# Kernel tuning notes

Measured on AMD Instinct MI355X. Metric: run time of the kernel, lower is better.

The kernel has to match this reference:

```python
import jax, jax.numpy as jnp
import numpy as np

N, E, P = 50000, 1600000, 500000
IN_DIM, HID, OUT = 512, 128, 64
EPS = 1e-5


def setup_inputs() -> dict:
    key = jax.random.key(0)
    ks = jax.random.split(key, 16)
    d = {}
    d['x'] = jax.random.normal(ks[0], (N, IN_DIM), dtype=jnp.float32)
    d['ei'] = jax.random.randint(ks[1], (2, E), 0, N, dtype=jnp.int32)
    d['src'] = jax.random.randint(ks[2], (P,), 0, N, dtype=jnp.int32)
    d['dst'] = jax.random.randint(ks[3], (P,), 0, N, dtype=jnp.int32)
    # GCNConv layer 1 params
    d['W1'] = jax.random.normal(ks[4], (IN_DIM, HID), dtype=jnp.float32) / np.sqrt(IN_DIM)
    d['b1'] = jnp.zeros((HID,), jnp.float32)
    d['bn1_gamma'] = jnp.ones((HID,), jnp.float32)
    d['bn1_beta'] = jnp.zeros((HID,), jnp.float32)
    d['bn1_mean'] = jnp.zeros((HID,), jnp.float32)
    d['bn1_var'] = jnp.ones((HID,), jnp.float32)
    # GCNConv layer 2 params
    d['W2'] = jax.random.normal(ks[5], (HID, OUT), dtype=jnp.float32) / np.sqrt(HID)
    d['b2'] = jnp.zeros((OUT,), jnp.float32)
    d['bn2_gamma'] = jnp.ones((OUT,), jnp.float32)
    d['bn2_beta'] = jnp.zeros((OUT,), jnp.float32)
    d['bn2_mean'] = jnp.zeros((OUT,), jnp.float32)
    d['bn2_var'] = jnp.ones((OUT,), jnp.float32)
    # edge head MLP
    d['hW1'] = jax.random.normal(ks[6], (2 * OUT, OUT), dtype=jnp.float32) / np.sqrt(2 * OUT)
    d['hb1'] = jnp.zeros((OUT,), jnp.float32)
    d['hW2'] = jax.random.normal(ks[7], (OUT, 1), dtype=jnp.float32) / np.sqrt(OUT)
    d['hb2'] = jnp.zeros((1,), jnp.float32)
    return d


def gcn_conv(x, ei, W, b):
    """PyG-style GCNConv: add self-loops, symmetric deg^-1/2 normalization."""
    xw = x @ W  # [N, F]
    row, col = ei[0], ei[1]
    ones = jnp.ones((ei.shape[1],), x.dtype)
    deg = jax.ops.segment_sum(ones, col, num_segments=N) + 1.0  # +1 for self-loop
    dinv = jax.lax.rsqrt(deg)
    norm = dinv[row] * dinv[col]  # [E]
    agg = jax.ops.segment_sum(norm[:, None] * xw[row], col, num_segments=N)
    # self-loop contribution: dinv[i]^2 * xw[i]
    return agg + (dinv * dinv)[:, None] * xw + b


def bn_eval(x, gamma, beta, mean, var):
    return (x - mean) * jax.lax.rsqrt(var + EPS) * gamma + beta


def reference(x, ei, src, dst, W1, b1, bn1_gamma, bn1_beta, bn1_mean, bn1_var,
              W2, b2, bn2_gamma, bn2_beta, bn2_mean, bn2_var, hW1, hb1, hW2, hb2):
    h = jax.nn.relu(bn_eval(gcn_conv(x, ei, W1, b1), bn1_gamma, bn1_beta, bn1_mean, bn1_var))
    # dropout is identity in eval mode
    z = jax.nn.relu(bn_eval(gcn_conv(h, ei, W2, b2), bn2_gamma, bn2_beta, bn2_mean, bn2_var))
    pair = jnp.concatenate([z[src], z[dst]], axis=1)  # [P, 2*OUT]
    hmid = jax.nn.relu(pair @ hW1 + hb1)
    logits = hmid @ hW2 + hb2  # [P, 1]
    return jax.nn.sigmoid(logits).squeeze(-1)
```

## Files before the change

### kernel.cpp

```cpp
#include <hip/hip_runtime.h>
#include <math.h>


typedef __attribute__((ext_vector_type(8))) short short8x;
typedef __attribute__((ext_vector_type(4))) float f32x4;

__device__ __forceinline__ unsigned short f2bf(float f) {
  unsigned int u = __float_as_uint(f);
  unsigned int r = u + 0x7FFFu + ((u >> 16) & 1u);
  return (unsigned short)(r >> 16);
}
__device__ __forceinline__ float bf2f(unsigned short u) {
  return __uint_as_float(((unsigned int)u) << 16);
}


__global__ void zero_int_kernel(int* __restrict__ p, int n) {
  int i = blockIdx.x * blockDim.x + threadIdx.x;
  if (i < n) p[i] = 0;
}

__global__ void degree_hist_kernel(const int* __restrict__ col, int* __restrict__ deg, int E) {
  int i = blockIdx.x * blockDim.x + threadIdx.x;
  if (i < E) atomicAdd(&deg[col[i]], 1);
}

__global__ __launch_bounds__(256) void scan_blocksum_kernel(const int* __restrict__ deg,
                                                            int* __restrict__ bsum, int n) {
  __shared__ int ws[4];
  int base = blockIdx.x * 1024;
  int tid = threadIdx.x;
  int s = 0;
#pragma unroll
  for (int j = 0; j < 4; ++j) {
    int i = base + tid + j * 256;
    if (i < n) s += deg[i];
  }
#pragma unroll
  for (int d = 1; d < 64; d <<= 1) s += __shfl_xor(s, d, 64);
  if ((tid & 63) == 0) ws[tid >> 6] = s;
  __syncthreads();
  if (tid == 0) bsum[blockIdx.x] = ws[0] + ws[1] + ws[2] + ws[3];
}

__global__ __launch_bounds__(64) void scan_bsum_kernel(int* __restrict__ bsum, int nb,
                                                       int* __restrict__ total) {
  int lane = threadIdx.x;
  int v = (lane < nb) ? bsum[lane] : 0;
  int incl = v;
#pragma unroll
  for (int d = 1; d < 64; d <<= 1) {
    int t = __shfl_up(incl, d, 64);
    if (lane >= d) incl += t;
  }
  if (lane < nb) bsum[lane] = incl - v;
  if (lane == 63) *total = incl;
}

__global__ __launch_bounds__(256) void scan_final_kernel(const int* __restrict__ deg,
                                                         const int* __restrict__ bsum,
                                                         int* __restrict__ offs,
                                                         float* __restrict__ dinv, int n) {
  __shared__ int wsum[4];
  int tid = threadIdx.x;
  int lane = tid & 63;
  int wid = tid >> 6;
  int idx0 = blockIdx.x * 1024 + tid * 4;
  int v[4];
#pragma unroll
  for (int j = 0; j < 4; ++j) {
    int i = idx0 + j;
    v[j] = (i < n) ? deg[i] : 0;
  }
  int tsum = v[0] + v[1] + v[2] + v[3];
  int incl = tsum;
#pragma unroll
  for (int d = 1; d < 64; d <<= 1) {
    int t = __shfl_up(incl, d, 64);
    if (lane >= d) incl += t;
  }
  if (lane == 63) wsum[wid] = incl;
  __syncthreads();
  int woff = 0;
#pragma unroll
  for (int w = 0; w < 4; ++w)
    if (w < wid) woff += wsum[w];
  int run = woff + incl - tsum + bsum[blockIdx.x];
#pragma unroll
  for (int j = 0; j < 4; ++j) {
    int i = idx0 + j;
    if (i < n) {
      offs[i] = run;
      dinv[i] = rsqrtf((float)v[j] + 1.0f);
      run += v[j];
    }
  }
}

__global__ void bucket_init_kernel(const int* __restrict__ offs, const int* __restrict__ total,
                                   int* __restrict__ bcur, int* __restrict__ offs_n, int NBK) {
  int b = blockIdx.x * blockDim.x + threadIdx.x;
  if (b < NBK) bcur[b] = offs[b * 256];
  if (b == 0) *offs_n = *total;
}

__global__ __launch_bounds__(256) void binA_kernel(const int* __restrict__ row,
                                                   const int* __restrict__ col,
                                                   int* __restrict__ bcur,
                                                   unsigned int* __restrict__ staging, int E,
                                                   int NBK) {
  __shared__ int hist[256];
  const int tid = threadIdx.x;
  hist[tid] = 0;
  __syncthreads();
  const int base = blockIdx.x * 4096;
  unsigned int payload[16];
  int bk[16];
#pragma unroll
  for (int j = 0; j < 16; ++j) {
    int i = base + j * 256 + tid;
    if (i < E) {
      unsigned int c = (unsigned int)col[i];
      unsigned int r = (unsigned int)row[i];
      payload[j] = (c << 16) | r;
      bk[j] = (int)(c >> 8);
      atomicAdd(&hist[bk[j]], 1);
    } else {
      bk[j] = -1;
    }
  }
  __syncthreads();
  if (tid < NBK) {
    int h = hist[tid];
    hist[tid] = h ? atomicAdd(&bcur[tid], h) : 0;
  }
  __syncthreads();
#pragma unroll
  for (int j = 0; j < 16; ++j) {
    if (bk[j] >= 0) {
      int p = atomicAdd(&hist[bk[j]], 1);
      staging[p] = payload[j];
    }
  }
}

__global__ __launch_bounds__(512) void binB_kernel(const unsigned int* __restrict__ staging,
                                                   const int* __restrict__ offs,
                                                   const float* __restrict__ dinv,
                                                   unsigned int* __restrict__ csr, int N) {
  __shared__ int cur[256];
  const int b = blockIdx.x;
  const int n0 = b * 256;
  const int nn = min(256, N - n0);
  const int tid = threadIdx.x;
  if (tid < nn) cur[tid] = offs[n0 + tid];
  __syncthreads();
  const int s = offs[n0];
  const int e = offs[min(n0 + 256, N)];
  for (int t = s + tid; t < e; t += 512) {
    unsigned int v = __builtin_nontemporal_load(&staging[t]);
    int cl = (int)((v >> 16) & 255u);
    unsigned int r = v & 0xFFFFu;
    unsigned int wd = f2bf(dinv[r]);
    int p = atomicAdd(&cur[cl], 1);
    csr[p] = (wd << 16) | r;
  }
}

__global__ void prep_bfrag_kernel(const float* __restrict__ W, unsigned short* __restrict__ out,
                                  int K, int N) {
  int idx = blockIdx.x * blockDim.x + threadIdx.x;
  int KS = K / 32;
  int total = (N / 16) * KS * 64;
  if (idx >= total) return;
  int lane = idx & 63;
  int t = idx >> 6;
  int ks = t % KS;
  int nt = t / KS;
  int n = nt * 16 + (lane & 15);
  int k0 = ks * 32 + (lane >> 4) * 8;
  unsigned short* o = out + (size_t)idx * 8;
#pragma unroll
  for (int j = 0; j < 8; ++j) o[j] = f2bf(W[(size_t)(k0 + j) * N + n]);
}

template <int K, int N, bool ABF16>
__global__ __launch_bounds__(256) void mfma_gemm_kernel(const void* __restrict__ Ap,
                                                        const unsigned short* __restrict__ Bfrag,
                                                        unsigned short* __restrict__ Cout, int M) {
  constexpr int KS = K / 32;
  constexpr int NT = N / 16;
  const int lane = threadIdx.x & 63;
  const int wid = threadIdx.x >> 6;
  const int quad = lane >> 4;
  const int lc = lane & 15;
  const int mbase = blockIdx.x * 128 + wid * 32;
  if (mbase >= M) return;

  f32x4 acc[2][NT];
#pragma unroll
  for (int mt = 0; mt < 2; ++mt)
#pragma unroll
    for (int nt = 0; nt < NT; ++nt) acc[mt][nt] = (f32x4){0.f, 0.f, 0.f, 0.f};

  int r0 = mbase + lc;
  int r1 = mbase + 16 + lc;
  if (r0 >= M) r0 = M - 1;
  if (r1 >= M) r1 = M - 1;

#pragma unroll
  for (int ks = 0; ks < KS; ++ks) {
    const int k0 = ks * 32 + quad * 8;
    short8x a[2];
    if constexpr (ABF16) {
      const unsigned short* A = (const unsigned short*)Ap;
      a[0] = *(const short8x*)(A + (size_t)r0 * K + k0);
      a[1] = *(const short8x*)(A + (size_t)r1 * K + k0);
    } else {
      const float* A = (const float*)Ap;
      const float4* p0 = (const float4*)(A + (size_t)r0 * K + k0);
      const float4* p1 = (const float4*)(A + (size_t)r1 * K + k0);
      float4 u0 = p0[0], v0 = p0[1];
      float4 u1 = p1[0], v1 = p1[1];
      short8x t0, t1;
      t0[0] = (short)f2bf(u0.x); t0[1] = (short)f2bf(u0.y);
      t0[2] = (short)f2bf(u0.z); t0[3] = (short)f2bf(u0.w);
      t0[4] = (short)f2bf(v0.x); t0[5] = (short)f2bf(v0.y);
      t0[6] = (short)f2bf(v0.z); t0[7] = (short)f2bf(v0.w);
      t1[0] = (short)f2bf(u1.x); t1[1] = (short)f2bf(u1.y);
      t1[2] = (short)f2bf(u1.z); t1[3] = (short)f2bf(u1.w);
      t1[4] = (short)f2bf(v1.x); t1[5] = (short)f2bf(v1.y);
      t1[6] = (short)f2bf(v1.z); t1[7] = (short)f2bf(v1.w);
      a[0] = t0;
      a[1] = t1;
    }
#pragma unroll
    for (int nt = 0; nt < NT; ++nt) {
      short8x b = *(const short8x*)(Bfrag + (((size_t)nt * KS + ks) * 64 + lane) * 8);
      acc[0][nt] = __builtin_amdgcn_mfma_f32_16x16x32_bf16(a[0], b, acc[0][nt], 0, 0, 0);
      acc[1][nt] = __builtin_amdgcn_mfma_f32_16x16x32_bf16(a[1], b, acc[1][nt], 0, 0, 0);
    }
  }

#pragma unroll
  for (int mt = 0; mt < 2; ++mt)
#pragma unroll
    for (int nt = 0; nt < NT; ++nt)
#pragma unroll
      for (int reg = 0; reg < 4; ++reg) {
        int row = mbase + mt * 16 + quad * 4 + reg;
        if (row < M) Cout[(size_t)row * N + nt * 16 + lc] = f2bf(acc[mt][nt][reg]);
      }
}

template <int F>
__global__ __launch_bounds__(256) void agg_fast_kernel(
    const unsigned short* __restrict__ xw, const int* __restrict__ offs,
    const unsigned int* __restrict__ csr, const float* __restrict__ dinv,
    const float* __restrict__ bias, const float* __restrict__ gamma,
    const float* __restrict__ beta, const float* __restrict__ mean,
    const float* __restrict__ var, unsigned short* __restrict__ out, int N) {
  constexpr int G = F / 2;
  constexpr int NPB = 256 / G;
  const int li = threadIdx.x % G;
  const int i = blockIdx.x * NPB + threadIdx.x / G;
  if (i >= N) return;
  const unsigned int* xw32 = (const unsigned int*)xw;
  const float di = dinv[i];
  const int s = offs[i], e = offs[i + 1];
  float accL = 0.f, accH = 0.f;
  int t = s;
  for (; t + 16 <= e; t += 16) {
    unsigned int ent[16];
#pragma unroll
    for (int j = 0; j < 16; ++j) ent[j] = csr[t + j];
    unsigned int gv[16];
#pragma unroll
    for (int j = 0; j < 16; ++j) gv[j] = xw32[(size_t)(ent[j] & 0xFFFFu) * G + li];
#pragma unroll
    for (int j = 0; j < 16; ++j) {
      float w = __uint_as_float(ent[j] & 0xFFFF0000u);
      accL += w * __uint_as_float(gv[j] << 16);
      accH += w * __uint_as_float(gv[j] & 0xFFFF0000u);
    }
  }
  for (; t + 4 <= e; t += 4) {
    unsigned int ent[4];
#pragma unroll
    for (int j = 0; j < 4; ++j) ent[j] = csr[t + j];
    unsigned int gv[4];
#pragma unroll
    for (int j = 0; j < 4; ++j) gv[j] = xw32[(size_t)(ent[j] & 0xFFFFu) * G + li];
#pragma unroll
    for (int j = 0; j < 4; ++j) {
      float w = __uint_as_float(ent[j] & 0xFFFF0000u);
      accL += w * __uint_as_float(gv[j] << 16);
      accH += w * __uint_as_float(gv[j] & 0xFFFF0000u);
    }
  }
  for (; t < e; ++t) {
    unsigned int ee = csr[t];
    unsigned int gv = xw32[(size_t)(ee & 0xFFFFu) * G + li];
    float w = __uint_as_float(ee & 0xFFFF0000u);
    accL += w * __uint_as_float(gv << 16);
    accH += w * __uint_as_float(gv & 0xFFFF0000u);
  }
  const int f0 = 2 * li, f1 = f0 + 1;
  unsigned int sv = xw32[(size_t)i * G + li];
  float v0 = di * accL + di * di * __uint_as_float(sv << 16) + bias[f0];
  float v1 = di * accH + di * di * __uint_as_float(sv & 0xFFFF0000u) + bias[f1];
  v0 = (v0 - mean[f0]) * rsqrtf(var[f0] + 1e-5f) * gamma[f0] + beta[f0];
  v1 = (v1 - mean[f1]) * rsqrtf(var[f1] + 1e-5f) * gamma[f1] + beta[f1];
  unsigned int packed =
      (unsigned int)f2bf(fmaxf(v0, 0.f)) | ((unsigned int)f2bf(fmaxf(v1, 0.f)) << 16);
  ((unsigned int*)out)[(size_t)i * G + li] = packed;
}

__global__ __launch_bounds__(256) void head_mfma_kernel(
    const unsigned short* __restrict__ z, const int* __restrict__ src,
    const int* __restrict__ dst, const unsigned short* __restrict__ bfragH,
    const float* __restrict__ hb1, const float* __restrict__ hw2,
    const float* __restrict__ hb2, float* __restrict__ out, int P) {
  const int lane = threadIdx.x & 63;
  const int quad = lane >> 4;
  const int lc = lane & 15;

  short8x bf[4][4];
#pragma unroll
  for (int nt = 0; nt < 4; ++nt)
#pragma unroll
    for (int ks = 0; ks < 4; ++ks)
      bf[nt][ks] = *(const short8x*)(bfragH + (((size_t)nt * 4 + ks) * 64 + lane) * 8);

  float b1v[4], w2v[4];
#pragma unroll
  for (int nt = 0; nt < 4; ++nt) {
    b1v[nt] = hb1[nt * 16 + lc];
    w2v[nt] = hw2[nt * 16 + lc];
  }
  const float bias2 = hb2[0];

  const int nchunks = (P + 15) / 16;
  const int gw = blockIdx.x * 4 + (threadIdx.x >> 6);
  const int nw = gridDim.x * 4;

  for (int ch = gw; ch < nchunks; ch += nw) {
    int p = ch * 16 + lc;
    int pc = p < P ? p : P - 1;
    int s = src[pc], d = dst[pc];
    const unsigned short* zs = z + (size_t)s * 64;
    const unsigned short* zd = z + (size_t)d * 64;
    short8x a[4];
    a[0] = *(const short8x*)(zs + quad * 8);
    a[1] = *(const short8x*)(zs + 32 + quad * 8);
    a[2] = *(const short8x*)(zd + quad * 8);
    a[3] = *(const short8x*)(zd + 32 + quad * 8);

    f32x4 acc[4];
#pragma unroll
    for (int nt = 0; nt < 4; ++nt) acc[nt] = (f32x4){0.f, 0.f, 0.f, 0.f};
#pragma unroll
    for (int nt = 0; nt < 4; ++nt)
#pragma unroll
      for (int t = 0; t < 4; ++t)
        acc[nt] = __builtin_amdgcn_mfma_f32_16x16x32_bf16(a[t], bf[nt][t], acc[nt], 0, 0, 0);

    float part[4];
#pragma unroll
    for (int reg = 0; reg < 4; ++reg) {
      float sum = 0.f;
#pragma unroll
      for (int nt = 0; nt < 4; ++nt) sum += fmaxf(acc[nt][reg] + b1v[nt], 0.f) * w2v[nt];
      part[reg] = sum;
    }
#pragma unroll
    for (int m = 1; m < 16; m <<= 1) {
#pragma unroll
      for (int reg = 0; reg < 4; ++reg) part[reg] += __shfl_xor(part[reg], m, 64);
    }
    if (lc == 0) {
      int pbase = ch * 16 + quad * 4;
      float4 o;
      o.x = 1.0f / (1.0f + __expf(-(part[0] + bias2)));
      o.y = 1.0f / (1.0f + __expf(-(part[1] + bias2)));
      o.z = 1.0f / (1.0f + __expf(-(part[2] + bias2)));
      o.w = 1.0f / (1.0f + __expf(-(part[3] + bias2)));
      if (pbase + 3 < P) {
        *(float4*)(out + pbase) = o;
      } else {
        float ov[4] = {o.x, o.y, o.z, o.w};
        for (int reg = 0; reg < 4; ++reg)
          if (pbase + reg < P) out[pbase + reg] = ov[reg];
      }
    }
  }
}


extern "C" void kernel_launch(void* const* d_in, const int* in_sizes, int n_in,
                              void* d_out, int out_size, void* d_ws, size_t ws_size,
                              hipStream_t stream) {
  const float* x = (const float*)d_in[0];
  const int* ei = (const int*)d_in[1];
  const int* src = (const int*)d_in[2];
  const int* dst = (const int*)d_in[3];
  const float* W1 = (const float*)d_in[4];
  const float* b1 = (const float*)d_in[5];
  const float* g1 = (const float*)d_in[6];
  const float* be1 = (const float*)d_in[7];
  const float* mu1 = (const float*)d_in[8];
  const float* va1 = (const float*)d_in[9];
  const float* W2 = (const float*)d_in[10];
  const float* b2 = (const float*)d_in[11];
  const float* g2 = (const float*)d_in[12];
  const float* be2 = (const float*)d_in[13];
  const float* mu2 = (const float*)d_in[14];
  const float* va2 = (const float*)d_in[15];
  const float* hW1 = (const float*)d_in[16];
  const float* hb1 = (const float*)d_in[17];
  const float* hW2 = (const float*)d_in[18];
  const float* hb2 = (const float*)d_in[19];
  float* out = (float*)d_out;

  const int N = in_sizes[0] / 512;
  const int E = in_sizes[1] / 2;
  const int P = in_sizes[2];
  const int* row = ei;
  const int* col = ei + E;
  const int NBK = (N + 255) / 256;
  const int NSB = (N + 1023) / 1024;
  const int NAB = (E + 4095) / 4096;

  char* wp = (char*)d_ws;
  auto alloc = [&](size_t bytes) {
    char* p = wp;
    wp += (bytes + 255) & ~(size_t)255;
    return p;
  };
  unsigned short* xw1 = (unsigned short*)alloc((size_t)N * 128 * 2);
  unsigned short* h = (unsigned short*)alloc((size_t)N * 128 * 2);
  unsigned short* xw2 = (unsigned short*)alloc((size_t)N * 64 * 2);
  unsigned short* z = (unsigned short*)alloc((size_t)N * 64 * 2);
  float* dinv = (float*)alloc((size_t)N * 4);
  int* deg = (int*)alloc((size_t)N * 4);
  int* offs = (int*)alloc((size_t)(N + 1) * 4);
  unsigned int* csr = (unsigned int*)alloc((size_t)E * 4);
  unsigned int* staging = (unsigned int*)alloc((size_t)E * 4);
  int* bsum = (int*)alloc((size_t)NSB * 4);
  int* bcur = (int*)alloc((size_t)NBK * 4);
  int* total = (int*)alloc(256);
  unsigned short* bfW1 = (unsigned short*)alloc(512 * 128 * 2);
  unsigned short* bfW2 = (unsigned short*)alloc(128 * 64 * 2);
  unsigned short* bfH = (unsigned short*)alloc(128 * 64 * 2);
  (void)ws_size;
  (void)n_in;
  (void)out_size;

  hipLaunchKernelGGL(zero_int_kernel, dim3((N + 255) / 256), dim3(256), 0, stream, deg, N);
  hipLaunchKernelGGL(degree_hist_kernel, dim3((E + 255) / 256), dim3(256), 0, stream, col, deg, E);
  hipLaunchKernelGGL(scan_blocksum_kernel, dim3(NSB), dim3(256), 0, stream, deg, bsum, N);
  hipLaunchKernelGGL(scan_bsum_kernel, dim3(1), dim3(64), 0, stream, bsum, NSB, total);
  hipLaunchKernelGGL(scan_final_kernel, dim3(NSB), dim3(256), 0, stream, deg, bsum, offs, dinv, N);
  hipLaunchKernelGGL(bucket_init_kernel, dim3((NBK + 255) / 256), dim3(256), 0, stream, offs, total,
                     bcur, offs + N, NBK);
  hipLaunchKernelGGL(binA_kernel, dim3(NAB), dim3(256), 0, stream, row, col, bcur, staging, E, NBK);
  hipLaunchKernelGGL(binB_kernel, dim3(NBK), dim3(512), 0, stream, staging, offs, dinv, csr, N);

  hipLaunchKernelGGL(prep_bfrag_kernel, dim3((8 * 16 * 64 + 255) / 256), dim3(256), 0, stream, W1,
                     bfW1, 512, 128);
  hipLaunchKernelGGL(prep_bfrag_kernel, dim3((4 * 4 * 64 + 255) / 256), dim3(256), 0, stream, W2,
                     bfW2, 128, 64);
  hipLaunchKernelGGL(prep_bfrag_kernel, dim3((4 * 4 * 64 + 255) / 256), dim3(256), 0, stream, hW1,
                     bfH, 128, 64);

  hipLaunchKernelGGL((mfma_gemm_kernel<512, 128, false>), dim3((N + 127) / 128), dim3(256), 0,
                     stream, x, bfW1, xw1, N);
  hipLaunchKernelGGL((agg_fast_kernel<128>), dim3((N + 3) / 4), dim3(256), 0, stream, xw1, offs,
                     csr, dinv, b1, g1, be1, mu1, va1, h, N);

  hipLaunchKernelGGL((mfma_gemm_kernel<128, 64, true>), dim3((N + 127) / 128), dim3(256), 0, stream,
                     h, bfW2, xw2, N);
  hipLaunchKernelGGL((agg_fast_kernel<64>), dim3((N + 7) / 8), dim3(256), 0, stream, xw2, offs,
                     csr, dinv, b2, g2, be2, mu2, va2, z, N);

  hipLaunchKernelGGL(head_mfma_kernel, dim3(2048), dim3(256), 0, stream, z, src, dst, bfH, hb1,
                     hW2, hb2, out, P);
}
```

Measured before the change: 439.1 us.

## Replace global degree histogram with bucket-level counting and per-bucket local degree scan

Removes the per-edge global atomic degree histogram and the node-level multi-kernel scan. Edges are now first counted per 256-node bucket with shared-memory histograms, a single-block scan gives bucket starts, and after scattering into staging each bucket block computes per-node degrees, offsets and dinv from its staged edges. The goal is to cut contended global atomics and launches, at the cost of an extra pass over col and one more pass over the staging buffer.

```diff
diff --git a/kernel.cpp b/kernel.cpp
--- a/kernel.cpp
+++ b/kernel.cpp
@@ -20,95 +20,64 @@
   if (i < n) p[i] = 0;
 }
 
-__global__ void degree_hist_kernel(const int* __restrict__ col, int* __restrict__ deg, int E) {
-  int i = blockIdx.x * blockDim.x + threadIdx.x;
-  if (i < E) atomicAdd(&deg[col[i]], 1);
-}
-
-__global__ __launch_bounds__(256) void scan_blocksum_kernel(const int* __restrict__ deg,
-                                                            int* __restrict__ bsum, int n) {
+__global__ __launch_bounds__(256) void binA_hist_kernel(const int* __restrict__ col,
+                                                        int* __restrict__ bucket_count, int E,
+                                                        int NBK) {
+  __shared__ int hist[256];
+  const int tid = threadIdx.x;
+  hist[tid] = 0;
+  __syncthreads();
+  const int base = blockIdx.x * 4096;
+#pragma unroll
+  for (int j = 0; j < 16; ++j) {
+    int i = base + j * 256 + tid;
+    if (i < E) atomicAdd(&hist[((unsigned int)col[i]) >> 8], 1);
+  }
+  __syncthreads();
+  if (tid < NBK) {
+    int h = hist[tid];
+    if (h) atomicAdd(&bucket_count[tid], h);
+  }
+}
+
+__global__ __launch_bounds__(256) void scan_buckets_kernel(const int* __restrict__ bucket_count,
+                                                           int* __restrict__ bucket_start,
+                                                           int* __restrict__ bcur,
+                                                           int* __restrict__ offs_n, int NBK,
+                                                           int E) {
   __shared__ int ws[4];
-  int base = blockIdx.x * 1024;
-  int tid = threadIdx.x;
-  int s = 0;
-#pragma unroll
-  for (int j = 0; j < 4; ++j) {
-    int i = base + tid + j * 256;
-    if (i < n) s += deg[i];
-  }
-#pragma unroll
-  for (int d = 1; d < 64; d <<= 1) s += __shfl_xor(s, d, 64);
-  if ((tid & 63) == 0) ws[tid >> 6] = s;
-  __syncthreads();
-  if (tid == 0) bsum[blockIdx.x] = ws[0] + ws[1] + ws[2] + ws[3];
-}
-
-__global__ __launch_bounds__(64) void scan_bsum_kernel(int* __restrict__ bsum, int nb,
-                                                       int* __restrict__ total) {
-  int lane = threadIdx.x;
-  int v = (lane < nb) ? bsum[lane] : 0;
+  const int tid = threadIdx.x;
+  const int lane = tid & 63;
+  const int wid = tid >> 6;
+  int v = (tid < NBK) ? bucket_count[tid] : 0;
   int incl = v;
 #pragma unroll
   for (int d = 1; d < 64; d <<= 1) {
     int t = __shfl_up(incl, d, 64);
     if (lane >= d) incl += t;
   }
-  if (lane < nb) bsum[lane] = incl - v;
-  if (lane == 63) *total = incl;
-}
-
-__global__ __launch_bounds__(256) void scan_final_kernel(const int* __restrict__ deg,
-                                                         const int* __restrict__ bsum,
-                                                         int* __restrict__ offs,
-                                                         float* __restrict__ dinv, int n) {
-  __shared__ int wsum[4];
-  int tid = threadIdx.x;
-  int lane = tid & 63;
-  int wid = tid >> 6;
-  int idx0 = blockIdx.x * 1024 + tid * 4;
-  int v[4];
-#pragma unroll
-  for (int j = 0; j < 4; ++j) {
-    int i = idx0 + j;
-    v[j] = (i < n) ? deg[i] : 0;
-  }
-  int tsum = v[0] + v[1] + v[2] + v[3];
-  int incl = tsum;
-#pragma unroll
-  for (int d = 1; d < 64; d <<= 1) {
-    int t = __shfl_up(incl, d, 64);
-    if (lane >= d) incl += t;
-  }
-  if (lane == 63) wsum[wid] = incl;
+  if (lane == 63) ws[wid] = incl;
   __syncthreads();
   int woff = 0;
 #pragma unroll
   for (int w = 0; w < 4; ++w)
-    if (w < wid) woff += wsum[w];
-  int run = woff + incl - tsum + bsum[blockIdx.x];
-#pragma unroll
-  for (int j = 0; j < 4; ++j) {
-    int i = idx0 + j;
-    if (i < n) {
-      offs[i] = run;
-      dinv[i] = rsqrtf((float)v[j] + 1.0f);
-      run += v[j];
-    }
-  }
-}
-
-__global__ void bucket_init_kernel(const int* __restrict__ offs, const int* __restrict__ total,
-                                   int* __restrict__ bcur, int* __restrict__ offs_n, int NBK) {
-  int b = blockIdx.x * blockDim.x + threadIdx.x;
-  if (b < NBK) bcur[b] = offs[b * 256];
-  if (b == 0) *offs_n = *total;
-}
-
-__global__ __launch_bounds__(256) void binA_kernel(const int* __restrict__ row,
-                                                   const int* __restrict__ col,
-                                                   int* __restrict__ bcur,
-                                                   unsigned int* __restrict__ staging, int E,
-                                                   int NBK) {
+    if (w < wid) woff += ws[w];
+  int excl = woff + incl - v;
+  if (tid < NBK) {
+    bucket_start[tid] = excl;
+    bcur[tid] = excl;
+  }
+  if (tid == 0) {
+    bucket_start[NBK] = E;
+    *offs_n = E;
+  }
+}
+
+__global__ __launch_bounds__(256) void binA_scatter_kernel(const int* __restrict__ row,
+                                                           const int* __restrict__ col,
+                                                           int* __restrict__ bcur,
+                                                           unsigned int* __restrict__ staging,
+                                                           int E, int NBK) {
   __shared__ int hist[256];
   const int tid = threadIdx.x;
   hist[tid] = 0;
@@ -144,19 +113,59 @@
   }
 }
 
-__global__ __launch_bounds__(512) void binB_kernel(const unsigned int* __restrict__ staging,
-                                                   const int* __restrict__ offs,
-                                                   const float* __restrict__ dinv,
-                                                   unsigned int* __restrict__ csr, int N) {
+__global__ __launch_bounds__(256) void binB1_kernel(const unsigned int* __restrict__ staging,
+                                                    const int* __restrict__ bucket_start,
+                                                    int* __restrict__ offs,
+                                                    float* __restrict__ dinv, int N) {
+  __shared__ int cnt[256];
+  __shared__ int ws[4];
+  const int b = blockIdx.x;
+  const int n0 = b * 256;
+  const int tid = threadIdx.x;
+  cnt[tid] = 0;
+  __syncthreads();
+  const int s = bucket_start[b];
+  const int e = bucket_start[b + 1];
+  for (int t = s + tid; t < e; t += 256) {
+    atomicAdd(&cnt[(staging[t] >> 16) & 255u], 1);
+  }
+  __syncthreads();
+  const int deg = cnt[tid];
+  const int lane = tid & 63;
+  const int wid = tid >> 6;
+  int incl = deg;
+#pragma unroll
+  for (int d = 1; d < 64; d <<= 1) {
+    int t = __shfl_up(incl, d, 64);
+    if (lane >= d) incl += t;
+  }
+  if (lane == 63) ws[wid] = incl;
+  __syncthreads();
+  int woff = 0;
+#pragma unroll
+  for (int w = 0; w < 4; ++w)
+    if (w < wid) woff += ws[w];
+  const int excl = woff + incl - deg;
+  const int node = n0 + tid;
+  if (node < N) {
+    offs[node] = s + excl;
+    dinv[node] = rsqrtf((float)deg + 1.0f);
+  }
+}
+
+__global__ __launch_bounds__(512) void binB2_kernel(const unsigned int* __restrict__ staging,
+                                                    const int* __restrict__ offs,
+                                                    const int* __restrict__ bucket_start,
+                                                    const float* __restrict__ dinv,
+                                                    unsigned int* __restrict__ csr, int N) {
   __shared__ int cur[256];
   const int b = blockIdx.x;
   const int n0 = b * 256;
-  const int nn = min(256, N - n0);
   const int tid = threadIdx.x;
-  if (tid < nn) cur[tid] = offs[n0 + tid];
-  __syncthreads();
-  const int s = offs[n0];
-  const int e = offs[min(n0 + 256, N)];
+  if (tid < 256 && n0 + tid < N) cur[tid] = offs[n0 + tid];
+  __syncthreads();
+  const int s = bucket_start[b];
+  const int e = bucket_start[b + 1];
   for (int t = s + tid; t < e; t += 512) {
     unsigned int v = __builtin_nontemporal_load(&staging[t]);
     int cl = (int)((v >> 16) & 255u);
@@ -428,7 +437,6 @@
   const int* row = ei;
   const int* col = ei + E;
   const int NBK = (N + 255) / 256;
-  const int NSB = (N + 1023) / 1024;
   const int NAB = (E + 4095) / 4096;
 
   char* wp = (char*)d_ws;
@@ -442,13 +450,12 @@
   unsigned short* xw2 = (unsigned short*)alloc((size_t)N * 64 * 2);
   unsigned short* z = (unsigned short*)alloc((size_t)N * 64 * 2);
   float* dinv = (float*)alloc((size_t)N * 4);
-  int* deg = (int*)alloc((size_t)N * 4);
   int* offs = (int*)alloc((size_t)(N + 1) * 4);
   unsigned int* csr = (unsigned int*)alloc((size_t)E * 4);
   unsigned int* staging = (unsigned int*)alloc((size_t)E * 4);
-  int* bsum = (int*)alloc((size_t)NSB * 4);
+  int* bucket_count = (int*)alloc((size_t)NBK * 4);
+  int* bucket_start = (int*)alloc((size_t)(NBK + 1) * 4);
   int* bcur = (int*)alloc((size_t)NBK * 4);
-  int* total = (int*)alloc(256);
   unsigned short* bfW1 = (unsigned short*)alloc(512 * 128 * 2);
   unsigned short* bfW2 = (unsigned short*)alloc(128 * 64 * 2);
   unsigned short* bfH = (unsigned short*)alloc(128 * 64 * 2);
@@ -456,15 +463,17 @@
   (void)n_in;
   (void)out_size;
 
-  hipLaunchKernelGGL(zero_int_kernel, dim3((N + 255) / 256), dim3(256), 0, stream, deg, N);
-  hipLaunchKernelGGL(degree_hist_kernel, dim3((E + 255) / 256), dim3(256), 0, stream, col, deg, E);
-  hipLaunchKernelGGL(scan_blocksum_kernel, dim3(NSB), dim3(256), 0, stream, deg, bsum, N);
-  hipLaunchKernelGGL(scan_bsum_kernel, dim3(1), dim3(64), 0, stream, bsum, NSB, total);
-  hipLaunchKernelGGL(scan_final_kernel, dim3(NSB), dim3(256), 0, stream, deg, bsum, offs, dinv, N);
-  hipLaunchKernelGGL(bucket_init_kernel, dim3((NBK + 255) / 256), dim3(256), 0, stream, offs, total,
-                     bcur, offs + N, NBK);
-  hipLaunchKernelGGL(binA_kernel, dim3(NAB), dim3(256), 0, stream, row, col, bcur, staging, E, NBK);
-  hipLaunchKernelGGL(binB_kernel, dim3(NBK), dim3(512), 0, stream, staging, offs, dinv, csr, N);
+  hipLaunchKernelGGL(zero_int_kernel, dim3((NBK + 255) / 256), dim3(256), 0, stream, bucket_count,
+                     NBK);
+  hipLaunchKernelGGL(binA_hist_kernel, dim3(NAB), dim3(256), 0, stream, col, bucket_count, E, NBK);
+  hipLaunchKernelGGL(scan_buckets_kernel, dim3(1), dim3(256), 0, stream, bucket_count,
+                     bucket_start, bcur, offs + N, NBK, E);
+  hipLaunchKernelGGL(binA_scatter_kernel, dim3(NAB), dim3(256), 0, stream, row, col, bcur, staging,
+                     E, NBK);
+  hipLaunchKernelGGL(binB1_kernel, dim3(NBK), dim3(256), 0, stream, staging, bucket_start, offs,
+                     dinv, N);
+  hipLaunchKernelGGL(binB2_kernel, dim3(NBK), dim3(512), 0, stream, staging, offs, bucket_start,
+                     dinv, csr, N);
 
   hipLaunchKernelGGL(prep_bfrag_kernel, dim3((8 * 16 * 64 + 255) / 256), dim3(256), 0, stream, W1,
                      bfW1, 512, 128);
```

Result: faster. 387.2 us (-11.8%).
